# Kernel optimization log

Hardware: AMD Instinct MI355X
Metric: run time of the kernel (lower is better)

The kernel has to match this reference:

```python
import jax, jax.numpy as jnp
import numpy as np

N_HEAD = 16
QMIN, QMAX = 0.0, 255.0  # 8-bit asymmetric


def fake_quantize(x, scale, zp):
    # LearnableFakeQuantize (asymmetric, 8-bit) with straight-through round.
    q = x / scale + zp
    q = q + jax.lax.stop_gradient(jnp.round(q) - q)  # STE round
    q = jnp.clip(q, QMIN, QMAX)
    return (q - zp) * scale


def setup_inputs() -> dict:
    key = jax.random.key(0)
    ks = jax.random.split(key, 4)
    B, T, C = 2, 2048, 1024
    return {
        "hidden_states": jax.random.normal(ks[0], (B, T, C), jnp.float32),
        "W_attn": jax.random.normal(ks[1], (C, 3 * C), jnp.float32) * (1.0 / np.sqrt(C)),
        "b_attn": jnp.zeros((3 * C,), jnp.float32),
        "W_proj": jax.random.normal(ks[2], (C, C), jnp.float32) * (1.0 / np.sqrt(C)),
        "b_proj": jnp.zeros((C,), jnp.float32),
        "kv_scale": jnp.full((1,), 0.05, jnp.float32),
        "kv_zp": jnp.full((1,), 128.0, jnp.float32),
    }


def reference(hidden_states, W_attn, b_attn, W_proj, b_proj, kv_scale, kv_zp):
    B, T, C = hidden_states.shape
    H = N_HEAD
    D = C // H
    qkv = hidden_states @ W_attn + b_attn            # [B,T,3C]
    q, k, v = jnp.split(qkv, 3, axis=2)
    # [B,T,C] -> [B,H,T,D]
    q = q.reshape(B, T, H, D).transpose(0, 2, 1, 3)
    k = k.reshape(B, T, H, D).transpose(0, 2, 1, 3)
    v = v.reshape(B, T, H, D).transpose(0, 2, 1, 3)
    k = fake_quantize(k, kv_scale, kv_zp)
    v = fake_quantize(v, kv_scale, kv_zp)
    scores = jnp.einsum("bhqd,bhkd->bhqk", q, k) / jnp.sqrt(jnp.asarray(D, q.dtype))
    causal = jnp.tril(jnp.ones((T, T), bool))        # bias[:T,:T]
    scores = jnp.where(causal, scores, jnp.asarray(-jnp.inf, scores.dtype))
    attn = jax.nn.softmax(scores, axis=-1)
    out = jnp.einsum("bhqk,bhkd->bhqd", attn, v)     # [B,H,T,D]
    out = out.transpose(0, 2, 1, 3).reshape(B, T, C)
    return out @ W_proj + b_proj
```

## Files before the change

### kernel.cpp

```cpp
#include <hip/hip_runtime.h>
#include <math.h>

#define TB 2048
#define CC 1024
#define NH 16
#define HD 64

typedef __bf16 bf16x8 __attribute__((ext_vector_type(8)));
typedef __bf16 bf16x4 __attribute__((ext_vector_type(4)));
typedef float  f32x4  __attribute__((ext_vector_type(4)));

__device__ inline float exp2fast(float x) { return __builtin_amdgcn_exp2f(x); }

__device__ __forceinline__ void gl_lds16(const __bf16* g, __bf16* l) {
    __builtin_amdgcn_global_load_lds(
        (const __attribute__((address_space(1))) void*)g,
        (__attribute__((address_space(3))) void*)l, 16, 0, 0);
}

__global__ __launch_bounds__(256)
void prep_kernel(const float* __restrict__ hidden, __bf16* __restrict__ hb,
                 const float* __restrict__ Wa, __bf16* __restrict__ wat,
                 const float* __restrict__ Wp, __bf16* __restrict__ wpt)
{
    __shared__ __bf16 L[64][68];
    const int tid = threadIdx.x;
    const int bid = blockIdx.x;
    if (bid < 4096) {
        int i = (bid * 256 + tid) * 4;
        f32x4 v = *(const f32x4*)&hidden[i];
        bf16x4 o;
        o.x = (__bf16)v.x; o.y = (__bf16)v.y; o.z = (__bf16)v.z; o.w = (__bf16)v.w;
        *(bf16x4*)&hb[i] = o;
        return;
    }
    const float* src; __bf16* dst; int N, n0, k0;
    if (bid < 4096 + 768) {
        int t = bid - 4096;
        src = Wa; dst = wat; N = 3072;
        n0 = (t % 48) * 64; k0 = (t / 48) * 64;
    } else {
        int t = bid - 4864;
        src = Wp; dst = wpt; N = 1024;
        n0 = (t % 16) * 64; k0 = (t / 16) * 64;
    }
    #pragma unroll
    for (int i = 0; i < 4; i++) {
        int id = tid + i * 256;
        int r = id >> 4, c = (id & 15) * 4;
        f32x4 v = *(const f32x4*)&src[(size_t)(k0 + r) * N + n0 + c];
        bf16x4 o;
        o.x = (__bf16)v.x; o.y = (__bf16)v.y; o.z = (__bf16)v.z; o.w = (__bf16)v.w;
        *(bf16x4*)&L[r][c] = o;
    }
    __syncthreads();
    #pragma unroll
    for (int i = 0; i < 4; i++) {
        int id = tid + i * 256;
        int nr = id >> 4, kc = (id & 15) * 4;
        bf16x4 o;
        o.x = L[kc + 0][nr]; o.y = L[kc + 1][nr];
        o.z = L[kc + 2][nr]; o.w = L[kc + 3][nr];
        *(bf16x4*)&dst[(size_t)(n0 + nr) * 1024 + k0 + kc] = o;
    }
}

template<int BN, int MODE>
__global__ __launch_bounds__(256)
void gemm_bt(const __bf16* __restrict__ A, const __bf16* __restrict__ Bt,
             const float* __restrict__ bias,
             __bf16* __restrict__ o0, __bf16* __restrict__ o1,
             __bf16* __restrict__ o2, float* __restrict__ of,
             int M, int N, int K,
             const float* __restrict__ scp, const float* __restrict__ zpp)
{
    constexpr int NT = BN / 32;
    __shared__ __bf16 Asm[128][64];
    __shared__ __bf16 Bsm[BN][64];

    const int tid  = threadIdx.x;
    const int m0   = blockIdx.y * 128;
    const int n0   = blockIdx.x * BN;
    const int w    = tid >> 6, lane = tid & 63;
    const int wm   = (w & 1) * 64, wn = (w >> 1) * (BN / 2);
    const int r16  = lane & 15, quad = lane >> 4;
    const int srow = lane >> 3;
    const int scol = ((lane & 7) ^ srow) * 8;
    const int rsw  = r16 & 7;

    f32x4 acc[NT][4];
    #pragma unroll
    for (int i = 0; i < NT; i++)
        #pragma unroll
        for (int j = 0; j < 4; j++) acc[i][j] = 0.f;

    for (int k0 = 0; k0 < K; k0 += 64) {
        #pragma unroll
        for (int p = 0; p < 4; p++)
            gl_lds16(&A[(size_t)(m0 + w * 32 + p * 8 + srow) * K + k0 + scol],
                     &Asm[w * 32 + p * 8][0]);
        #pragma unroll
        for (int p = 0; p < BN / 32; p++)
            gl_lds16(&Bt[(size_t)(n0 + w * (BN / 4) + p * 8 + srow) * K + k0 + scol],
                     &Bsm[w * (BN / 4) + p * 8][0]);
        __syncthreads();

        #pragma unroll
        for (int ks = 0; ks < 2; ks++) {
            const int col = ((ks * 4 + quad) ^ rsw) * 8;
            bf16x8 af[4], bfr[NT];
            #pragma unroll
            for (int mt = 0; mt < 4; mt++)
                af[mt] = *(const bf16x8*)&Asm[wm + mt * 16 + r16][col];
            #pragma unroll
            for (int nt = 0; nt < NT; nt++)
                bfr[nt] = *(const bf16x8*)&Bsm[wn + nt * 16 + r16][col];
            #pragma unroll
            for (int nt = 0; nt < NT; nt++)
                #pragma unroll
                for (int mt = 0; mt < 4; mt++)
                    acc[nt][mt] = __builtin_amdgcn_mfma_f32_16x16x32_bf16(
                        bfr[nt], af[mt], acc[nt][mt], 0, 0, 0);
        }
        __syncthreads();
    }

    const float sc = scp[0];
    const float zp = zpp[0];

    #pragma unroll
    for (int nt = 0; nt < NT; nt++) {
        #pragma unroll
        for (int mt = 0; mt < 4; mt++) {
            int gm = m0 + wm + mt * 16 + r16;
            int gn = n0 + wn + nt * 16 + quad * 4;
            f32x4 val = acc[nt][mt] + *(const f32x4*)&bias[gn];
            if (MODE == 1) {
                *(f32x4*)&of[(size_t)gm * N + gn] = val;
            } else {
                int part = gn >> 10;
                int idx  = gn & 1023;
                int h = idx >> 6, d = idx & 63;
                int b = gm >> 11, t = gm & 2047;
                size_t off = (((size_t)(b * NH + h)) * TB + t) * HD + d;
                bf16x4 st;
                if (part == 0) {
                    #pragma unroll
                    for (int r = 0; r < 4; r++)
                        st[r] = (__bf16)(val[r] * 0.18033688f);
                    *(bf16x4*)&o0[off] = st;
                } else {
                    #pragma unroll
                    for (int r = 0; r < 4; r++) {
                        float qv = val[r] / sc + zp;
                        qv = rintf(qv);
                        qv = fminf(fmaxf(qv, 0.f), 255.f);
                        st[r] = (__bf16)((qv - zp) * sc);
                    }
                    if (part == 1) *(bf16x4*)&o1[off] = st;
                    else           *(bf16x4*)&o2[off] = st;
                }
            }
        }
    }
}

__global__ __launch_bounds__(512, 4)
void attn_mfma(const __bf16* __restrict__ Q, const __bf16* __restrict__ Kg,
               const __bf16* __restrict__ Vg, __bf16* __restrict__ O)
{
    __shared__ alignas(16) __bf16 Ksm[64][72];
    __shared__ alignas(16) __bf16 Vsm[64][72];

    const int tid  = threadIdx.x;
    const int p    = blockIdx.x >> 5;
    const int bh   = blockIdx.x & 31;
    const int w    = tid >> 6, lane = tid & 63;
    const int wq   = w & 3;
    const int qt   = (w < 4) ? (31 - p) : p;
    const int ktmax = 31 - p;
    const int q0   = qt * 64;
    const int l15  = lane & 15, quad = lane >> 4;
    const int b    = bh >> 4, h = bh & 15;

    const int krow = tid >> 3;
    const int kseg = (tid & 7) * 8;
    const int vkey = tid & 63;
    const int vc   = tid >> 6;

    const __bf16* Kbh = Kg + (size_t)bh * TB * HD;
    const __bf16* Vbh = Vg + (size_t)bh * TB * HD;

    const __bf16* Qrow = Q + ((size_t)bh * TB + q0 + wq * 16 + l15) * HD;
    bf16x8 qf0 = *(const bf16x8*)&Qrow[quad * 8];
    bf16x8 qf1 = *(const bf16x8*)&Qrow[32 + quad * 8];

    const int rbase = (l15 >> 2) * 8 + (l15 & 3);

    bf16x8 af_l;
    {
        __bf16 v = (l15 == 0) ? (__bf16)1.0f : (__bf16)0.0f;
        #pragma unroll
        for (int j = 0; j < 8; j++) af_l[j] = v;
    }

    f32x4 acc_o[4], acc_l;
    #pragma unroll
    for (int nt = 0; nt < 4; nt++) acc_o[nt] = 0.f;
    acc_l = 0.f;
    float mrun = -3.0e38f;

    bf16x8 kpre = *(const bf16x8*)&Kbh[(size_t)krow * HD + kseg];
    bf16x8 vpre = *(const bf16x8*)&Vbh[(size_t)vkey * HD + vc * 8];

    for (int kt = 0; kt <= ktmax; kt++) {
        __syncthreads();
        *(bf16x8*)&Ksm[krow][kseg] = kpre;
        #pragma unroll
        for (int j = 0; j < 8; j++)
            Vsm[vc * 8 + j][vkey] = vpre[j];
        __syncthreads();

        if (kt < ktmax) {
            const __bf16* Kn = Kbh + (size_t)(kt + 1) * 64 * HD;
            const __bf16* Vn = Vbh + (size_t)(kt + 1) * 64 * HD;
            kpre = *(const bf16x8*)&Kn[(size_t)krow * HD + kseg];
            vpre = *(const bf16x8*)&Vn[(size_t)vkey * HD + vc * 8];
        }

        if (kt > qt) continue;

        const bool diag = (kt == qt);

        f32x4 s[4];
        #pragma unroll
        for (int nt = 0; nt < 4; nt++) s[nt] = 0.f;
        __builtin_amdgcn_s_setprio(1);
        #pragma unroll
        for (int nt = 0; nt < 4; nt++) {
            if (diag && (nt & 1) && wq < 2) continue;
            int row = rbase + (nt & 1) * 32 + ((nt >> 1) << 2);
            bf16x8 kf0 = *(const bf16x8*)&Ksm[row][quad * 8];
            bf16x8 kf1 = *(const bf16x8*)&Ksm[row][32 + quad * 8];
            s[nt] = __builtin_amdgcn_mfma_f32_16x16x32_bf16(kf0, qf0, s[nt], 0, 0, 0);
            s[nt] = __builtin_amdgcn_mfma_f32_16x16x32_bf16(kf1, qf1, s[nt], 0, 0, 0);
        }
        __builtin_amdgcn_s_setprio(0);

        if (diag) {
            #pragma unroll
            for (int nt = 0; nt < 4; nt++) {
                int koff = (nt & 1) * 32 + ((nt >> 1) << 2) + quad * 8;
                #pragma unroll
                for (int r = 0; r < 4; r++)
                    if (koff + r > wq * 16 + l15) s[nt][r] = -3.0e38f;
            }
        }

        float m0 = fmaxf(fmaxf(s[0][0], s[0][1]), fmaxf(s[0][2], s[0][3]));
        float m1 = fmaxf(fmaxf(s[1][0], s[1][1]), fmaxf(s[1][2], s[1][3]));
        float m2 = fmaxf(fmaxf(s[2][0], s[2][1]), fmaxf(s[2][2], s[2][3]));
        float m3 = fmaxf(fmaxf(s[3][0], s[3][1]), fmaxf(s[3][2], s[3][3]));
        float mx = fmaxf(fmaxf(m0, m1), fmaxf(m2, m3));
        mx = fmaxf(mx, __shfl_xor(mx, 16));
        mx = fmaxf(mx, __shfl_xor(mx, 32));

        if (__any((mx - mrun) > 8.0f)) {
            float mnew  = fmaxf(mrun, mx);
            float alpha = exp2fast(mrun - mnew);
            mrun = mnew;
            #pragma unroll
            for (int nt = 0; nt < 4; nt++)
                #pragma unroll
                for (int r = 0; r < 4; r++) acc_o[nt][r] *= alpha;
            acc_l[0] *= alpha;
        }

        float pv[4][4];
        #pragma unroll
        for (int nt = 0; nt < 4; nt++)
            #pragma unroll
            for (int r = 0; r < 4; r++) pv[nt][r] = exp2fast(s[nt][r] - mrun);

        bf16x8 pf0, pf1;
        #pragma unroll
        for (int j = 0; j < 4; j++) {
            pf0[j]     = (__bf16)pv[0][j];
            pf0[4 + j] = (__bf16)pv[2][j];
            pf1[j]     = (__bf16)pv[1][j];
            pf1[4 + j] = (__bf16)pv[3][j];
        }

        __builtin_amdgcn_s_setprio(1);
        acc_l = __builtin_amdgcn_mfma_f32_16x16x32_bf16(af_l, pf0, acc_l, 0, 0, 0);
        acc_l = __builtin_amdgcn_mfma_f32_16x16x32_bf16(af_l, pf1, acc_l, 0, 0, 0);

        #pragma unroll
        for (int nt = 0; nt < 4; nt++) {
            bf16x8 vf0 = *(const bf16x8*)&Vsm[nt * 16 + l15][quad * 8];
            bf16x8 vf1 = *(const bf16x8*)&Vsm[nt * 16 + l15][32 + quad * 8];
            acc_o[nt] = __builtin_amdgcn_mfma_f32_16x16x32_bf16(vf0, pf0, acc_o[nt], 0, 0, 0);
            acc_o[nt] = __builtin_amdgcn_mfma_f32_16x16x32_bf16(vf1, pf1, acc_o[nt], 0, 0, 0);
        }
        __builtin_amdgcn_s_setprio(0);
    }

    float lall = __shfl(acc_l[0], l15);
    float inv  = 1.f / lall;
    size_t trow = (size_t)(b * TB) + q0 + wq * 16 + l15;
    #pragma unroll
    for (int nt = 0; nt < 4; nt++) {
        bf16x4 st;
        #pragma unroll
        for (int r = 0; r < 4; r++) st[r] = (__bf16)(acc_o[nt][r] * inv);
        *(bf16x4*)&O[trow * CC + h * HD + nt * 16 + quad * 4] = st;
    }
}

extern "C" void kernel_launch(void* const* d_in, const int* in_sizes, int n_in,
                              void* d_out, int out_size, void* d_ws, size_t ws_size,
                              hipStream_t stream) {
    (void)in_sizes; (void)n_in; (void)out_size; (void)ws_size;
    const float* hidden   = (const float*)d_in[0];
    const float* W_attn   = (const float*)d_in[1];
    const float* b_attn   = (const float*)d_in[2];
    const float* W_proj   = (const float*)d_in[3];
    const float* b_proj   = (const float*)d_in[4];
    const float* kv_scale = (const float*)d_in[5];
    const float* kv_zp    = (const float*)d_in[6];
    float* out = (float*)d_out;

    __bf16* hb  = (__bf16*)d_ws;
    __bf16* wat = hb  + (size_t)4096 * 1024;
    __bf16* wpt = wat + (size_t)3072 * 1024;
    __bf16* qws = wpt + (size_t)1024 * 1024;
    __bf16* kws = qws + (size_t)2 * NH * TB * HD;
    __bf16* vws = kws + (size_t)2 * NH * TB * HD;
    __bf16* ows = vws + (size_t)2 * NH * TB * HD;

    prep_kernel<<<5120, 256, 0, stream>>>(hidden, hb, W_attn, wat, W_proj, wpt);

    gemm_bt<128, 0><<<dim3(24, 32), 256, 0, stream>>>(
        hb, wat, b_attn, qws, kws, vws, nullptr, 4096, 3072, 1024, kv_scale, kv_zp);

    attn_mfma<<<dim3(16 * 32), 512, 0, stream>>>(qws, kws, vws, ows);

    gemm_bt<64, 1><<<dim3(16, 32), 256, 0, stream>>>(
        ows, wpt, b_proj, nullptr, nullptr, nullptr, out, 4096, 1024, 1024,
        kv_scale, kv_zp);
}
```

Baseline: 181.0 us.

## Load K directly into swizzled LDS and process two KV tiles per barrier pair

Result: no change. 182.5 us (+0.8%).

```diff
diff --git a/kernel.cpp b/kernel.cpp
--- a/kernel.cpp
+++ b/kernel.cpp
@@ -169,8 +169,8 @@
 void attn_mfma(const __bf16* __restrict__ Q, const __bf16* __restrict__ Kg,
                const __bf16* __restrict__ Vg, __bf16* __restrict__ O)
 {
-    __shared__ alignas(16) __bf16 Ksm[64][72];
-    __shared__ alignas(16) __bf16 Vsm[64][72];
+    __shared__ alignas(16) __bf16 Ksm[128][64];
+    __shared__ alignas(16) __bf16 Vsm[2][64][72];
 
     const int tid  = threadIdx.x;
     const int p    = blockIdx.x >> 5;
@@ -183,8 +183,8 @@
     const int l15  = lane & 15, quad = lane >> 4;
     const int b    = bh >> 4, h = bh & 15;
 
-    const int krow = tid >> 3;
-    const int kseg = (tid & 7) * 8;
+    const int krow8  = w * 8 + (lane >> 3);
+    const int ksegsw = (((lane & 7) ^ ((lane >> 3) & 3))) * 8;
     const int vkey = tid & 63;
     const int vc   = tid >> 6;
 
@@ -196,6 +196,7 @@
     bf16x8 qf1 = *(const bf16x8*)&Qrow[32 + quad * 8];
 
     const int rbase = (l15 >> 2) * 8 + (l15 & 3);
+    const int csw   = (quad ^ (l15 & 3)) * 8;
 
     bf16x8 af_l;
     {
@@ -210,26 +211,10 @@
     acc_l = 0.f;
     float mrun = -3.0e38f;
 
-    bf16x8 kpre = *(const bf16x8*)&Kbh[(size_t)krow * HD + kseg];
-    bf16x8 vpre = *(const bf16x8*)&Vbh[(size_t)vkey * HD + vc * 8];
-
-    for (int kt = 0; kt <= ktmax; kt++) {
-        __syncthreads();
-        *(bf16x8*)&Ksm[krow][kseg] = kpre;
-        #pragma unroll
-        for (int j = 0; j < 8; j++)
-            Vsm[vc * 8 + j][vkey] = vpre[j];
-        __syncthreads();
-
-        if (kt < ktmax) {
-            const __bf16* Kn = Kbh + (size_t)(kt + 1) * 64 * HD;
-            const __bf16* Vn = Vbh + (size_t)(kt + 1) * 64 * HD;
-            kpre = *(const bf16x8*)&Kn[(size_t)krow * HD + kseg];
-            vpre = *(const bf16x8*)&Vn[(size_t)vkey * HD + vc * 8];
-        }
-
-        if (kt > qt) continue;
-
+    bf16x8 vpreA = *(const bf16x8*)&Vbh[(size_t)vkey * HD + vc * 8];
+    bf16x8 vpreB = *(const bf16x8*)&Vbh[(size_t)(64 + vkey) * HD + vc * 8];
+
+    auto compute_tile = [&](int sel, int kt) {
         const bool diag = (kt == qt);
 
         f32x4 s[4];
@@ -239,9 +224,9 @@
         #pragma unroll
         for (int nt = 0; nt < 4; nt++) {
             if (diag && (nt & 1) && wq < 2) continue;
-            int row = rbase + (nt & 1) * 32 + ((nt >> 1) << 2);
-            bf16x8 kf0 = *(const bf16x8*)&Ksm[row][quad * 8];
-            bf16x8 kf1 = *(const bf16x8*)&Ksm[row][32 + quad * 8];
+            int row = sel * 64 + rbase + (nt & 1) * 32 + ((nt >> 1) << 2);
+            bf16x8 kf0 = *(const bf16x8*)&Ksm[row][csw];
+            bf16x8 kf1 = *(const bf16x8*)&Ksm[row][32 + csw];
             s[nt] = __builtin_amdgcn_mfma_f32_16x16x32_bf16(kf0, qf0, s[nt], 0, 0, 0);
             s[nt] = __builtin_amdgcn_mfma_f32_16x16x32_bf16(kf1, qf1, s[nt], 0, 0, 0);
         }
@@ -297,12 +282,44 @@
 
         #pragma unroll
         for (int nt = 0; nt < 4; nt++) {
-            bf16x8 vf0 = *(const bf16x8*)&Vsm[nt * 16 + l15][quad * 8];
-            bf16x8 vf1 = *(const bf16x8*)&Vsm[nt * 16 + l15][32 + quad * 8];
+            bf16x8 vf0 = *(const bf16x8*)&Vsm[sel][nt * 16 + l15][quad * 8];
+            bf16x8 vf1 = *(const bf16x8*)&Vsm[sel][nt * 16 + l15][32 + quad * 8];
             acc_o[nt] = __builtin_amdgcn_mfma_f32_16x16x32_bf16(vf0, pf0, acc_o[nt], 0, 0, 0);
             acc_o[nt] = __builtin_amdgcn_mfma_f32_16x16x32_bf16(vf1, pf1, acc_o[nt], 0, 0, 0);
         }
         __builtin_amdgcn_s_setprio(0);
+    };
+
+    for (int kt0 = 0; kt0 <= ktmax; kt0 += 2) {
+        const bool hasB = (kt0 + 1 <= ktmax);
+
+        __syncthreads();
+
+        gl_lds16(&Kbh[(size_t)(kt0 * 64 + krow8) * HD + ksegsw], &Ksm[w * 8][0]);
+        if (hasB)
+            gl_lds16(&Kbh[(size_t)((kt0 + 1) * 64 + krow8) * HD + ksegsw],
+                     &Ksm[64 + w * 8][0]);
+
+        #pragma unroll
+        for (int j = 0; j < 8; j++)
+            Vsm[0][vc * 8 + j][vkey] = vpreA[j];
+        if (hasB) {
+            #pragma unroll
+            for (int j = 0; j < 8; j++)
+                Vsm[1][vc * 8 + j][vkey] = vpreB[j];
+        }
+
+        __syncthreads();
+
+        {
+            int ta = kt0 + 2 <= ktmax ? kt0 + 2 : ktmax;
+            int tb = kt0 + 3 <= ktmax ? kt0 + 3 : ktmax;
+            vpreA = *(const bf16x8*)&Vbh[((size_t)ta * 64 + vkey) * HD + vc * 8];
+            vpreB = *(const bf16x8*)&Vbh[((size_t)tb * 64 + vkey) * HD + vc * 8];
+        }
+
+        if (kt0 <= qt)     compute_tile(0, kt0);
+        if (kt0 + 1 <= qt) compute_tile(1, kt0 + 1);
     }
 
     float lall = __shfl(acc_l[0], l15);
```

## Store V transposed in QKV epilogue and read K/V directly from global in attention

Applied to the files above, without the earlier changes.

After: 260.2 us. 43.8% more time.

```diff
diff --git a/kernel.cpp b/kernel.cpp
--- a/kernel.cpp
+++ b/kernel.cpp
@@ -142,14 +142,16 @@
                 int idx  = gn & 1023;
                 int h = idx >> 6, d = idx & 63;
                 int b = gm >> 11, t = gm & 2047;
-                size_t off = (((size_t)(b * NH + h)) * TB + t) * HD + d;
-                bf16x4 st;
                 if (part == 0) {
+                    size_t off = (((size_t)(b * NH + h)) * TB + t) * HD + d;
+                    bf16x4 st;
                     #pragma unroll
                     for (int r = 0; r < 4; r++)
                         st[r] = (__bf16)(val[r] * 0.18033688f);
                     *(bf16x4*)&o0[off] = st;
-                } else {
+                } else if (part == 1) {
+                    size_t off = (((size_t)(b * NH + h)) * TB + t) * HD + d;
+                    bf16x4 st;
                     #pragma unroll
                     for (int r = 0; r < 4; r++) {
                         float qv = val[r] / sc + zp;
@@ -157,8 +159,16 @@
                         qv = fminf(fmaxf(qv, 0.f), 255.f);
                         st[r] = (__bf16)((qv - zp) * sc);
                     }
-                    if (part == 1) *(bf16x4*)&o1[off] = st;
-                    else           *(bf16x4*)&o2[off] = st;
+                    *(bf16x4*)&o1[off] = st;
+                } else {
+                    #pragma unroll
+                    for (int r = 0; r < 4; r++) {
+                        float qv = val[r] / sc + zp;
+                        qv = rintf(qv);
+                        qv = fminf(fmaxf(qv, 0.f), 255.f);
+                        size_t offT = (((size_t)(b * NH + h)) * HD + d + r) * TB + t;
+                        o2[offT] = (__bf16)((qv - zp) * sc);
+                    }
                 }
             }
         }
@@ -167,29 +177,20 @@
 
 __global__ __launch_bounds__(512, 4)
 void attn_mfma(const __bf16* __restrict__ Q, const __bf16* __restrict__ Kg,
-               const __bf16* __restrict__ Vg, __bf16* __restrict__ O)
+               const __bf16* __restrict__ VgT, __bf16* __restrict__ O)
 {
-    __shared__ alignas(16) __bf16 Ksm[64][72];
-    __shared__ alignas(16) __bf16 Vsm[64][72];
-
     const int tid  = threadIdx.x;
     const int p    = blockIdx.x >> 5;
     const int bh   = blockIdx.x & 31;
     const int w    = tid >> 6, lane = tid & 63;
     const int wq   = w & 3;
     const int qt   = (w < 4) ? (31 - p) : p;
-    const int ktmax = 31 - p;
     const int q0   = qt * 64;
     const int l15  = lane & 15, quad = lane >> 4;
     const int b    = bh >> 4, h = bh & 15;
 
-    const int krow = tid >> 3;
-    const int kseg = (tid & 7) * 8;
-    const int vkey = tid & 63;
-    const int vc   = tid >> 6;
-
-    const __bf16* Kbh = Kg + (size_t)bh * TB * HD;
-    const __bf16* Vbh = Vg + (size_t)bh * TB * HD;
+    const __bf16* Kbh = Kg  + (size_t)bh * TB * HD;
+    const __bf16* Vbh = VgT + (size_t)bh * HD * TB;
 
     const __bf16* Qrow = Q + ((size_t)bh * TB + q0 + wq * 16 + l15) * HD;
     bf16x8 qf0 = *(const bf16x8*)&Qrow[quad * 8];
@@ -210,27 +211,10 @@
     acc_l = 0.f;
     float mrun = -3.0e38f;
 
-    bf16x8 kpre = *(const bf16x8*)&Kbh[(size_t)krow * HD + kseg];
-    bf16x8 vpre = *(const bf16x8*)&Vbh[(size_t)vkey * HD + vc * 8];
-
-    for (int kt = 0; kt <= ktmax; kt++) {
-        __syncthreads();
-        *(bf16x8*)&Ksm[krow][kseg] = kpre;
-        #pragma unroll
-        for (int j = 0; j < 8; j++)
-            Vsm[vc * 8 + j][vkey] = vpre[j];
-        __syncthreads();
-
-        if (kt < ktmax) {
-            const __bf16* Kn = Kbh + (size_t)(kt + 1) * 64 * HD;
-            const __bf16* Vn = Vbh + (size_t)(kt + 1) * 64 * HD;
-            kpre = *(const bf16x8*)&Kn[(size_t)krow * HD + kseg];
-            vpre = *(const bf16x8*)&Vn[(size_t)vkey * HD + vc * 8];
-        }
-
-        if (kt > qt) continue;
-
+    for (int kt = 0; kt <= qt; kt++) {
         const bool diag = (kt == qt);
+        const __bf16* Kt = Kbh + (size_t)kt * 64 * HD;
+        const __bf16* Vt = Vbh + (size_t)kt * 64;
 
         f32x4 s[4];
         #pragma unroll
@@ -240,12 +224,19 @@
         for (int nt = 0; nt < 4; nt++) {
             if (diag && (nt & 1) && wq < 2) continue;
             int row = rbase + (nt & 1) * 32 + ((nt >> 1) << 2);
-            bf16x8 kf0 = *(const bf16x8*)&Ksm[row][quad * 8];
-            bf16x8 kf1 = *(const bf16x8*)&Ksm[row][32 + quad * 8];
+            bf16x8 kf0 = *(const bf16x8*)&Kt[(size_t)row * HD + quad * 8];
+            bf16x8 kf1 = *(const bf16x8*)&Kt[(size_t)row * HD + 32 + quad * 8];
             s[nt] = __builtin_amdgcn_mfma_f32_16x16x32_bf16(kf0, qf0, s[nt], 0, 0, 0);
             s[nt] = __builtin_amdgcn_mfma_f32_16x16x32_bf16(kf1, qf1, s[nt], 0, 0, 0);
         }
         __builtin_amdgcn_s_setprio(0);
+
+        bf16x8 vf0[4], vf1[4];
+        #pragma unroll
+        for (int nt = 0; nt < 4; nt++) {
+            vf0[nt] = *(const bf16x8*)&Vt[(size_t)(nt * 16 + l15) * TB + quad * 8];
+            vf1[nt] = *(const bf16x8*)&Vt[(size_t)(nt * 16 + l15) * TB + 32 + quad * 8];
+        }
 
         if (diag) {
             #pragma unroll
@@ -297,10 +288,8 @@
 
         #pragma unroll
         for (int nt = 0; nt < 4; nt++) {
-            bf16x8 vf0 = *(const bf16x8*)&Vsm[nt * 16 + l15][quad * 8];
-            bf16x8 vf1 = *(const bf16x8*)&Vsm[nt * 16 + l15][32 + quad * 8];
-            acc_o[nt] = __builtin_amdgcn_mfma_f32_16x16x32_bf16(vf0, pf0, acc_o[nt], 0, 0, 0);
-            acc_o[nt] = __builtin_amdgcn_mfma_f32_16x16x32_bf16(vf1, pf1, acc_o[nt], 0, 0, 0);
+            acc_o[nt] = __builtin_amdgcn_mfma_f32_16x16x32_bf16(vf0[nt], pf0, acc_o[nt], 0, 0, 0);
+            acc_o[nt] = __builtin_amdgcn_mfma_f32_16x16x32_bf16(vf1[nt], pf1, acc_o[nt], 0, 0, 0);
         }
         __builtin_amdgcn_s_setprio(0);
     }
```

## Replace QKV GEMM with 256x256-tile kernel using multi-stage direct-to-LDS pipeline

Applied to the files above, without the earlier changes.

After: 185.1 us. 1.02x slower.

```diff
diff --git a/kernel.cpp b/kernel.cpp
--- a/kernel.cpp
+++ b/kernel.cpp
@@ -62,6 +62,140 @@
         o.x = L[kc + 0][nr]; o.y = L[kc + 1][nr];
         o.z = L[kc + 2][nr]; o.w = L[kc + 3][nr];
         *(bf16x4*)&dst[(size_t)(n0 + nr) * 1024 + k0 + kc] = o;
+    }
+}
+
+__global__ __launch_bounds__(512, 2)
+void gemm_qkv(const __bf16* __restrict__ A, const __bf16* __restrict__ Bt,
+              const float* __restrict__ bias,
+              __bf16* __restrict__ o0, __bf16* __restrict__ o1,
+              __bf16* __restrict__ o2,
+              const float* __restrict__ scp, const float* __restrict__ zpp)
+{
+    constexpr int K = 1024;
+    __shared__ __bf16 LA[4][256][32];
+    __shared__ __bf16 LB[4][256][32];
+
+    const int tid  = threadIdx.x;
+    const int wg   = blockIdx.x;
+    const int swzb = (wg & 7) * 24 + (wg >> 3);
+    const int m0   = (swzb / 12) * 256;
+    const int n0   = (swzb % 12) * 256;
+
+    const int w    = tid >> 6, lane = tid & 63;
+    const int wmi  = w >> 2;
+    const int wni  = w & 3;
+    const int r16  = lane & 15, quad = lane >> 4;
+
+    const int srow = lane >> 2;
+    const int scol = ((lane & 3) ^ (srow & 3)) * 8;
+
+    auto stageA = [&](int slot, int t) {
+        #pragma unroll
+        for (int c = 0; c < 2; c++)
+            gl_lds16(&A[(size_t)(m0 + c * 128 + w * 16 + srow) * K + t * 32 + scol],
+                     &LA[slot][c * 128 + w * 16][0]);
+    };
+    auto stageB = [&](int slot, int t) {
+        #pragma unroll
+        for (int c = 0; c < 2; c++)
+            gl_lds16(&Bt[(size_t)(n0 + c * 128 + w * 16 + srow) * K + t * 32 + scol],
+                     &LB[slot][c * 128 + w * 16][0]);
+    };
+
+    f32x4 acc[8][4];
+    #pragma unroll
+    for (int i = 0; i < 8; i++)
+        #pragma unroll
+        for (int j = 0; j < 4; j++) acc[i][j] = 0.f;
+
+    const float sc = scp[0];
+    const float zp = zpp[0];
+    f32x4 bias_r[4];
+    #pragma unroll
+    for (int nt = 0; nt < 4; nt++)
+        bias_r[nt] = *(const f32x4*)&bias[n0 + wni * 64 + nt * 16 + quad * 4];
+    asm volatile("s_waitcnt vmcnt(0)" ::: "memory");
+
+    stageA(0, 0); stageB(0, 0);
+    stageA(1, 1); stageB(1, 1);
+    stageA(2, 2); stageB(2, 2);
+    asm volatile("s_waitcnt vmcnt(8)" ::: "memory");
+    __builtin_amdgcn_s_barrier();
+
+    const int colr = (quad ^ (r16 & 3)) * 8;
+
+    for (int t = 0; t < 32; t++) {
+        const int slot = t & 3;
+        bf16x8 af[4], bfv[4];
+
+        #pragma unroll
+        for (int nt = 0; nt < 4; nt++)
+            bfv[nt] = *(const bf16x8*)&LB[slot][wni * 64 + nt * 16 + r16][colr];
+        #pragma unroll
+        for (int m = 0; m < 4; m++)
+            af[m] = *(const bf16x8*)&LA[slot][wmi * 128 + m * 16 + r16][colr];
+        if (t <= 28) stageA((t + 3) & 3, t + 3);
+        __builtin_amdgcn_s_barrier();
+        __builtin_amdgcn_s_setprio(1);
+        #pragma unroll
+        for (int nt = 0; nt < 4; nt++)
+            #pragma unroll
+            for (int m = 0; m < 4; m++)
+                acc[m][nt] = __builtin_amdgcn_mfma_f32_16x16x32_bf16(
+                    bfv[nt], af[m], acc[m][nt], 0, 0, 0);
+        __builtin_amdgcn_s_setprio(0);
+        __builtin_amdgcn_s_barrier();
+
+        #pragma unroll
+        for (int m = 0; m < 4; m++)
+            af[m] = *(const bf16x8*)&LA[slot][wmi * 128 + 64 + m * 16 + r16][colr];
+        if (t <= 28) stageB((t + 3) & 3, t + 3);
+        if (t <= 28)      asm volatile("s_waitcnt vmcnt(8)" ::: "memory");
+        else if (t == 29) asm volatile("s_waitcnt vmcnt(4)" ::: "memory");
+        else if (t == 30) asm volatile("s_waitcnt vmcnt(0)" ::: "memory");
+        __builtin_amdgcn_s_barrier();
+        __builtin_amdgcn_s_setprio(1);
+        #pragma unroll
+        for (int nt = 0; nt < 4; nt++)
+            #pragma unroll
+            for (int m = 0; m < 4; m++)
+                acc[4 + m][nt] = __builtin_amdgcn_mfma_f32_16x16x32_bf16(
+                    bfv[nt], af[m], acc[4 + m][nt], 0, 0, 0);
+        __builtin_amdgcn_s_setprio(0);
+        __builtin_amdgcn_s_barrier();
+    }
+
+    #pragma unroll
+    for (int nt = 0; nt < 4; nt++) {
+        #pragma unroll
+        for (int mt = 0; mt < 8; mt++) {
+            int gm = m0 + wmi * 128 + mt * 16 + r16;
+            int gn = n0 + wni * 64 + nt * 16 + quad * 4;
+            f32x4 val = acc[mt][nt] + bias_r[nt];
+            int part = gn >> 10;
+            int idx  = gn & 1023;
+            int h = idx >> 6, d = idx & 63;
+            int b = gm >> 11, t = gm & 2047;
+            size_t off = (((size_t)(b * NH + h)) * TB + t) * HD + d;
+            bf16x4 st;
+            if (part == 0) {
+                #pragma unroll
+                for (int r = 0; r < 4; r++)
+                    st[r] = (__bf16)(val[r] * 0.18033688f);
+                *(bf16x4*)&o0[off] = st;
+            } else {
+                #pragma unroll
+                for (int r = 0; r < 4; r++) {
+                    float qv = val[r] / sc + zp;
+                    qv = rintf(qv);
+                    qv = fminf(fmaxf(qv, 0.f), 255.f);
+                    st[r] = (__bf16)((qv - zp) * sc);
+                }
+                if (part == 1) *(bf16x4*)&o1[off] = st;
+                else           *(bf16x4*)&o2[off] = st;
+            }
+        }
     }
 }
 
@@ -340,8 +474,8 @@
 
     prep_kernel<<<5120, 256, 0, stream>>>(hidden, hb, W_attn, wat, W_proj, wpt);
 
-    gemm_bt<128, 0><<<dim3(24, 32), 256, 0, stream>>>(
-        hb, wat, b_attn, qws, kws, vws, nullptr, 4096, 3072, 1024, kv_scale, kv_zp);
+    gemm_qkv<<<192, 512, 0, stream>>>(
+        hb, wat, b_attn, qws, kws, vws, kv_scale, kv_zp);
 
     attn_mfma<<<dim3(16 * 32), 512, 0, stream>>>(qws, kws, vws, ows);
 
```
